# Kernel optimization log

Hardware: AMD Instinct MI355X
Metric: run time of the kernel (lower is better)

## Reference

```python
import jax, jax.numpy as jnp
import numpy as np

N_NODES = 100000
N_EDGES = 3200000
N_FEAT = 500
N_HID = 256
N_CLASS = 40


def spmm(edge_row, edge_col, edge_val, x, num_nodes):
    # out[i] = sum_{e: row[e]==i} val[e] * x[col[e]]
    msgs = edge_val[:, None] * x[edge_col]          # [E, F] gather + scale
    return jax.ops.segment_sum(msgs, edge_row, num_segments=num_nodes)


def setup_inputs() -> dict:
    key = jax.random.key(0)
    k1, k2, k3, k4, k5, k6, k7, k8 = jax.random.split(key, 8)
    features = jax.random.normal(k1, (N_NODES, N_FEAT), dtype=jnp.float32)
    edge_row = jax.random.randint(k2, (N_EDGES,), 0, N_NODES, dtype=jnp.int32)
    edge_col = jax.random.randint(k3, (N_EDGES,), 0, N_NODES, dtype=jnp.int32)
    edge_val = jax.random.uniform(k4, (N_EDGES,), dtype=jnp.float32)
    # Xavier-uniform linear weights, zero biases (as in reset_parameters)
    lim1 = float(np.sqrt(6.0 / (N_FEAT + N_HID)))
    W1 = jax.random.uniform(k5, (N_FEAT, N_HID), minval=-lim1, maxval=lim1, dtype=jnp.float32)
    b1 = jnp.zeros((N_HID,), dtype=jnp.float32)
    lim2 = float(np.sqrt(6.0 / (N_HID + N_CLASS)))
    W2 = jax.random.uniform(k6, (N_HID, N_CLASS), minval=-lim2, maxval=lim2, dtype=jnp.float32)
    b2 = jnp.zeros((N_CLASS,), dtype=jnp.float32)
    return {
        "features": features,
        "edge_row": edge_row,
        "edge_col": edge_col,
        "edge_val": edge_val,
        "W1": W1, "b1": b1, "W2": W2, "b2": b2,
    }


def reference(features, edge_row, edge_col, edge_val, W1, b1, W2, b2):
    # Layer 1: linear -> spmm -> relu   (eval mode: dropout is identity)
    h = features @ W1 + b1                          # [N, nhid]
    h = spmm(edge_row, edge_col, edge_val, h, N_NODES)
    h = jax.nn.relu(h)
    # Layer 2: linear -> spmm
    o = h @ W2 + b2                                 # [N, nclass]
    o = spmm(edge_row, edge_col, edge_val, o, N_NODES)
    return jax.nn.log_softmax(o, axis=1)
```

## Files before the change

kernel.cpp:

```cpp
#include <hip/hip_runtime.h>
#include <hip/hip_bf16.h>
#include <math.h>

#define N_NODES 100000
#define N_FEAT 500
#define N_HID 256
#define N_CLASS 40

typedef float f32x4 __attribute__((ext_vector_type(4)));
typedef int i32x4 __attribute__((ext_vector_type(4)));
typedef short short8 __attribute__((ext_vector_type(8)));
typedef unsigned short u16x8 __attribute__((ext_vector_type(8)));

__device__ __forceinline__ float b2f(unsigned short u) {
  union { unsigned int i; float f; } c; c.i = ((unsigned int)u) << 16; return c.f;
}
__device__ __forceinline__ unsigned short f2bu(float x) {
  __hip_bfloat16 b = __float2bfloat16(x);
  union { __hip_bfloat16 b; unsigned short u; } c; c.b = b; return c.u;
}
__device__ __forceinline__ void gload_lds16(const void* gptr, void* lptr) {
  __builtin_amdgcn_global_load_lds(
      (const __attribute__((address_space(1))) unsigned int*)gptr,
      (__attribute__((address_space(3))) unsigned int*)lptr, 16, 0, 0);
}

__global__ __launch_bounds__(256) void cast_w1(
    const float* __restrict__ W1, unsigned short* __restrict__ Bsw) {
  int t = blockIdx.x * 256 + threadIdx.x;
  int col = t >> 6, ch = t & 63;
  int g = ch >> 3, c = ch & 7;
  int c_src = c ^ (col & 7);
  int k = g * 64 + c_src * 8;
  u16x8 o;
#pragma unroll
  for (int j = 0; j < 8; j++) {
    int kk = k + j;
    o[j] = (kk < N_FEAT) ? f2bu(W1[(size_t)kk * N_HID + col]) : (unsigned short)0;
  }
  *(u16x8*)(Bsw + (size_t)col * 512 + g * 64 + c * 8) = o;
}

__global__ __launch_bounds__(512) void gemm1_mfma(
    const float* __restrict__ A, const unsigned short* __restrict__ Bsw,
    const float* __restrict__ b1, unsigned short* __restrict__ H, int M) {
  __shared__ __align__(16) char smem[49152];
  char* sA = smem;
  char* sB = smem + 16384;
  int tid = threadIdx.x;
  int lane = tid & 63, w = tid >> 6;
  int wr = w >> 2, wc = w & 3;
  int bm = blockIdx.x * 128;

  f32x4 acc[4][4];
#pragma unroll
  for (int m = 0; m < 4; m++)
#pragma unroll
    for (int n = 0; n < 4; n++) acc[m][n] = (f32x4)0.f;

  for (int s = 0; s < 8; s++) {
    int k0 = s * 64;
#pragma unroll
    for (int i = 0; i < 4; i++) {
      int f4 = i * 512 + tid;
      int row = f4 >> 4, cidx = f4 & 15;
      int grow = bm + row;
      int k = k0 + cidx * 4;
      float4 v = make_float4(0.f, 0.f, 0.f, 0.f);
      if (grow < M && k < N_FEAT) v = *(const float4*)(A + (size_t)grow * N_FEAT + k);
      ushort4 u;
      u.x = f2bu(v.x); u.y = f2bu(v.y); u.z = f2bu(v.z); u.w = f2bu(v.w);
      int chunk = cidx >> 1, sub = cidx & 1;
      int byte = row * 128 + (((chunk ^ (row & 7))) << 4) + (sub << 3);
      *(ushort4*)(sA + byte) = u;
    }
#pragma unroll
    for (int j = 0; j < 4; j++) {
      int base = j * 8192 + w * 1024;
      int L = base + lane * 16;
      int col = L >> 7, c = (L >> 4) & 7;
      const char* g = (const char*)Bsw + (size_t)col * 1024 + s * 128 + c * 16;
      gload_lds16(g, sB + base);
    }
    __syncthreads();
#pragma unroll
    for (int kk = 0; kk < 2; kk++) {
      int cw = kk * 4 + (lane >> 4);
      short8 af[4], bg[4];
#pragma unroll
      for (int m = 0; m < 4; m++) {
        int ar = wr * 64 + m * 16 + (lane & 15);
        af[m] = *(const short8*)(sA + ar * 128 + ((cw ^ (ar & 7)) << 4));
      }
#pragma unroll
      for (int n = 0; n < 4; n++) {
        int bc = wc * 64 + n * 16 + (lane & 15);
        bg[n] = *(const short8*)(sB + bc * 128 + ((cw ^ (bc & 7)) << 4));
      }
#pragma unroll
      for (int m = 0; m < 4; m++)
#pragma unroll
        for (int n = 0; n < 4; n++)
          acc[m][n] = __builtin_amdgcn_mfma_f32_16x16x32_bf16(af[m], bg[n], acc[m][n], 0, 0, 0);
    }
    __syncthreads();
  }

  float bias[4];
#pragma unroll
  for (int n = 0; n < 4; n++) bias[n] = b1[wc * 64 + n * 16 + (lane & 15)];
#pragma unroll
  for (int m = 0; m < 4; m++) {
#pragma unroll
    for (int r = 0; r < 4; r++) {
      int row = bm + wr * 64 + m * 16 + ((lane >> 4) << 2) + r;
      if (row < M) {
#pragma unroll
        for (int n = 0; n < 4; n++) {
          int col = wc * 64 + n * 16 + (lane & 15);
          H[(size_t)row * N_HID + col] = f2bu(acc[m][n][r] + bias[n]);
        }
      }
    }
  }
}

__global__ __launch_bounds__(256) void hist_kernel(
    const int* __restrict__ er, int* __restrict__ cnt, int E) {
  int nv = E >> 2;
  int t = blockIdx.x * 256 + threadIdx.x;
  int nthr = gridDim.x * 256;
  const i32x4* er4 = (const i32x4*)er;
  for (int i = t; i < nv; i += nthr) {
    i32x4 r = __builtin_nontemporal_load(&er4[i]);
    atomicAdd(&cnt[r.x], 1);
    atomicAdd(&cnt[r.y], 1);
    atomicAdd(&cnt[r.z], 1);
    atomicAdd(&cnt[r.w], 1);
  }
  int tail = nv << 2;
  if (blockIdx.x == 0 && threadIdx.x < E - tail)
    atomicAdd(&cnt[er[tail + threadIdx.x]], 1);
}

__global__ __launch_bounds__(1024) void scan1_kernel(
    int* __restrict__ cnt, int* __restrict__ bsum, int n) {
  __shared__ int wsum[16];
  int tid = threadIdx.x, lane = tid & 63, wid = tid >> 6;
  int i = blockIdx.x * 1024 + tid;
  int v = (i < n) ? cnt[i] : 0;
  int x = v;
#pragma unroll
  for (int off = 1; off < 64; off <<= 1) {
    int t = __shfl_up(x, off);
    if (lane >= off) x += t;
  }
  if (lane == 63) wsum[wid] = x;
  __syncthreads();
  if (tid < 16) {
    int ws = wsum[tid];
#pragma unroll
    for (int off = 1; off < 16; off <<= 1) {
      int t = __shfl_up(ws, off);
      if (tid >= off) ws += t;
    }
    wsum[tid] = ws;
  }
  __syncthreads();
  int excl = (wid ? wsum[wid - 1] : 0) + x - v;
  if (i < n) cnt[i] = excl;
  if (tid == 0) bsum[blockIdx.x] = wsum[15];
}

__global__ __launch_bounds__(64) void scan2_kernel(
    int* __restrict__ bsum, int* __restrict__ row_ptr, int nb, int n) {
  int lane = threadIdx.x;
  int carry = 0;
  for (int base = 0; base < nb; base += 64) {
    int i = base + lane;
    int v = (i < nb) ? bsum[i] : 0;
    int x = v;
#pragma unroll
    for (int off = 1; off < 64; off <<= 1) {
      int t = __shfl_up(x, off);
      if (lane >= off) x += t;
    }
    if (i < nb) bsum[i] = carry + x - v;
    carry += __shfl(x, 63);
  }
  if (lane == 0) row_ptr[n] = carry;
}

__global__ __launch_bounds__(256) void scan3_kernel(
    int* __restrict__ cnt, const int* __restrict__ bsum,
    int* __restrict__ row_ptr, int n) {
  int i = blockIdx.x * 256 + threadIdx.x;
  if (i >= n) return;
  int v = cnt[i] + bsum[i >> 10];
  cnt[i] = v;
  row_ptr[i] = v;
}

__global__ __launch_bounds__(256) void scatter_kernel(
    const int* __restrict__ er, const int* __restrict__ ec,
    const float* __restrict__ ev, int* __restrict__ cursor,
    int2* __restrict__ cv, int E) {
  int s = blockIdx.x & 7;
  int g = blockIdx.x >> 3;
  int ngrp = gridDim.x >> 3;
  int t = g * 256 + threadIdx.x;
  int nthr = ngrp * 256;
  int nv = E >> 2;
  const i32x4* er4 = (const i32x4*)er;
  const i32x4* ec4 = (const i32x4*)ec;
  const f32x4* ev4 = (const f32x4*)ev;
  for (int i = t; i < nv; i += nthr) {
    i32x4 r = __builtin_nontemporal_load(&er4[i]);
    i32x4 c = __builtin_nontemporal_load(&ec4[i]);
    f32x4 v = __builtin_nontemporal_load(&ev4[i]);
    if (((r.x >> 9) & 7) == s) {
      int p = atomicAdd(&cursor[r.x], 1);
      cv[p] = make_int2(c.x, __float_as_int(v.x));
    }
    if (((r.y >> 9) & 7) == s) {
      int p = atomicAdd(&cursor[r.y], 1);
      cv[p] = make_int2(c.y, __float_as_int(v.y));
    }
    if (((r.z >> 9) & 7) == s) {
      int p = atomicAdd(&cursor[r.z], 1);
      cv[p] = make_int2(c.z, __float_as_int(v.z));
    }
    if (((r.w >> 9) & 7) == s) {
      int p = atomicAdd(&cursor[r.w], 1);
      cv[p] = make_int2(c.w, __float_as_int(v.w));
    }
  }
  int tail = nv << 2;
  if (blockIdx.x == 0 && threadIdx.x < E - tail) {
    int i = tail + threadIdx.x;
    int row = er[i];
    int p = atomicAdd(&cursor[row], 1);
    cv[p] = make_int2(ec[i], __float_as_int(ev[i]));
  }
}

__global__ __launch_bounds__(256) void spmm_csr_256(
    const int* __restrict__ row_ptr, const int2* __restrict__ cv,
    const unsigned short* __restrict__ X, unsigned short* __restrict__ Y, int M) {
  int wave = (blockIdx.x * 256 + threadIdx.x) >> 6;
  int lane = threadIdx.x & 63;
  if (wave >= M) return;
  int start = row_ptr[wave], end = row_ptr[wave + 1];
  float a0 = 0.f, a1 = 0.f, a2 = 0.f, a3 = 0.f;
  const unsigned short* Xl = X + (lane << 2);
  int e = start;
  for (; e + 4 <= end; e += 4) {
    int2 p0 = cv[e], p1 = cv[e + 1], p2 = cv[e + 2], p3 = cv[e + 3];
    ushort4 x0 = *(const ushort4*)(Xl + (size_t)p0.x * N_HID);
    ushort4 x1 = *(const ushort4*)(Xl + (size_t)p1.x * N_HID);
    ushort4 x2 = *(const ushort4*)(Xl + (size_t)p2.x * N_HID);
    ushort4 x3 = *(const ushort4*)(Xl + (size_t)p3.x * N_HID);
    float v0 = __int_as_float(p0.y), v1 = __int_as_float(p1.y);
    float v2 = __int_as_float(p2.y), v3 = __int_as_float(p3.y);
    a0 = fmaf(v0, b2f(x0.x), a0); a1 = fmaf(v0, b2f(x0.y), a1);
    a2 = fmaf(v0, b2f(x0.z), a2); a3 = fmaf(v0, b2f(x0.w), a3);
    a0 = fmaf(v1, b2f(x1.x), a0); a1 = fmaf(v1, b2f(x1.y), a1);
    a2 = fmaf(v1, b2f(x1.z), a2); a3 = fmaf(v1, b2f(x1.w), a3);
    a0 = fmaf(v2, b2f(x2.x), a0); a1 = fmaf(v2, b2f(x2.y), a1);
    a2 = fmaf(v2, b2f(x2.z), a2); a3 = fmaf(v2, b2f(x2.w), a3);
    a0 = fmaf(v3, b2f(x3.x), a0); a1 = fmaf(v3, b2f(x3.y), a1);
    a2 = fmaf(v3, b2f(x3.z), a2); a3 = fmaf(v3, b2f(x3.w), a3);
  }
  for (; e < end; e++) {
    int2 p0 = cv[e];
    float v0 = __int_as_float(p0.y);
    ushort4 x0 = *(const ushort4*)(Xl + (size_t)p0.x * N_HID);
    a0 = fmaf(v0, b2f(x0.x), a0); a1 = fmaf(v0, b2f(x0.y), a1);
    a2 = fmaf(v0, b2f(x0.z), a2); a3 = fmaf(v0, b2f(x0.w), a3);
  }
  ushort4 o;
  o.x = f2bu(fmaxf(a0, 0.f)); o.y = f2bu(fmaxf(a1, 0.f));
  o.z = f2bu(fmaxf(a2, 0.f)); o.w = f2bu(fmaxf(a3, 0.f));
  *(ushort4*)(Y + (size_t)wave * N_HID + (lane << 2)) = o;
}

__global__ __launch_bounds__(256) void gemm2_kernel(
    const unsigned short* __restrict__ H, const float* __restrict__ W2,
    const float* __restrict__ b2, unsigned short* __restrict__ O, int M) {
  __shared__ float Ws[N_HID * N_CLASS];
  __shared__ float sb2[N_CLASS];
  int tid = threadIdx.x;
  for (int i = tid; i < N_HID * N_CLASS; i += 256) Ws[i] = W2[i];
  if (tid < N_CLASS) sb2[tid] = b2[tid];
  __syncthreads();
  int r0 = (blockIdx.x * 256 + tid) * 2;
  if (r0 >= M) return;
  int r1 = r0 + 1;
  bool has1 = r1 < M;
  float acc0[N_CLASS], acc1[N_CLASS];
#pragma unroll
  for (int n = 0; n < N_CLASS; n++) { acc0[n] = sb2[n]; acc1[n] = sb2[n]; }
  const unsigned short* h0 = H + (size_t)r0 * N_HID;
  const unsigned short* h1 = H + (size_t)(has1 ? r1 : r0) * N_HID;
  for (int k0 = 0; k0 < N_HID; k0 += 8) {
    u16x8 va = *(const u16x8*)(h0 + k0);
    u16x8 vb = *(const u16x8*)(h1 + k0);
#pragma unroll
    for (int j = 0; j < 8; j++) {
      float a0 = b2f(va[j]), a1 = b2f(vb[j]);
      const float* wrow = &Ws[(k0 + j) * N_CLASS];
#pragma unroll
      for (int n = 0; n < N_CLASS; n++) {
        float wv = wrow[n];
        acc0[n] = fmaf(a0, wv, acc0[n]);
        acc1[n] = fmaf(a1, wv, acc1[n]);
      }
    }
  }
  unsigned short* o0 = O + (size_t)r0 * N_CLASS;
#pragma unroll
  for (int n = 0; n < N_CLASS; n += 4) {
    ushort4 p;
    p.x = f2bu(acc0[n]); p.y = f2bu(acc0[n + 1]);
    p.z = f2bu(acc0[n + 2]); p.w = f2bu(acc0[n + 3]);
    *(ushort4*)(o0 + n) = p;
  }
  if (has1) {
    unsigned short* o1 = O + (size_t)r1 * N_CLASS;
#pragma unroll
    for (int n = 0; n < N_CLASS; n += 4) {
      ushort4 p;
      p.x = f2bu(acc1[n]); p.y = f2bu(acc1[n + 1]);
      p.z = f2bu(acc1[n + 2]); p.w = f2bu(acc1[n + 3]);
      *(ushort4*)(o1 + n) = p;
    }
  }
}

__global__ __launch_bounds__(256) void spmm_csr_40_lsm(
    const int* __restrict__ row_ptr, const int2* __restrict__ cv,
    const unsigned short* __restrict__ X, float* __restrict__ Out, int M) {
  int wave = (blockIdx.x * 256 + threadIdx.x) >> 6;
  int lane = threadIdx.x & 63;
  if (wave >= M) return;
  int start = row_ptr[wave], end = row_ptr[wave + 1];
  bool act = lane < N_CLASS;
  int ln = act ? lane : 0;
  const unsigned short* Xc = X + ln;
  float acc = 0.f;
  int e = start;
  for (; e + 4 <= end; e += 4) {
    int2 p0 = cv[e], p1 = cv[e + 1], p2 = cv[e + 2], p3 = cv[e + 3];
    unsigned short x0 = Xc[(size_t)p0.x * N_CLASS];
    unsigned short x1 = Xc[(size_t)p1.x * N_CLASS];
    unsigned short x2 = Xc[(size_t)p2.x * N_CLASS];
    unsigned short x3 = Xc[(size_t)p3.x * N_CLASS];
    acc = fmaf(__int_as_float(p0.y), b2f(x0), acc);
    acc = fmaf(__int_as_float(p1.y), b2f(x1), acc);
    acc = fmaf(__int_as_float(p2.y), b2f(x2), acc);
    acc = fmaf(__int_as_float(p3.y), b2f(x3), acc);
  }
  for (; e < end; e++) {
    int2 p0 = cv[e];
    acc = fmaf(__int_as_float(p0.y), b2f(Xc[(size_t)p0.x * N_CLASS]), acc);
  }
  float mv = act ? acc : -INFINITY;
#pragma unroll
  for (int off = 32; off; off >>= 1) mv = fmaxf(mv, __shfl_xor(mv, off));
  float ex = act ? expf(acc - mv) : 0.f;
  float s = ex;
#pragma unroll
  for (int off = 32; off; off >>= 1) s += __shfl_xor(s, off);
  float lse = mv + logf(s);
  if (act) Out[(size_t)wave * N_CLASS + lane] = acc - lse;
}

extern "C" void kernel_launch(void* const* d_in, const int* in_sizes, int n_in,
                              void* d_out, int out_size, void* d_ws, size_t ws_size,
                              hipStream_t stream) {
  const float* feat = (const float*)d_in[0];
  const int* er     = (const int*)d_in[1];
  const int* ec     = (const int*)d_in[2];
  const float* ev   = (const float*)d_in[3];
  const float* W1   = (const float*)d_in[4];
  const float* b1   = (const float*)d_in[5];
  const float* W2   = (const float*)d_in[6];
  const float* b2   = (const float*)d_in[7];
  float* out = (float*)d_out;
  const int M = N_NODES;
  const int E = in_sizes[1];

  char* ws = (char*)d_ws;
  unsigned short* h     = (unsigned short*)(ws);
  unsigned short* hpost = (unsigned short*)(ws + 51200000);
  unsigned short* o     = (unsigned short*)(ws + 102400000);
  int* row_ptr          = (int*)(ws + 110400000);
  int* cursor           = (int*)(ws + 110800016);
  int* bsum             = (int*)(ws + 111200032);
  int2* cv              = (int2*)(ws + 111200576);
  unsigned short* W1Tsw = (unsigned short*)(ws + 136800576);

  const int NB1 = (M + 1023) / 1024;

  cast_w1<<<64, 256, 0, stream>>>(W1, W1Tsw);
  (void)hipMemsetAsync(cursor, 0, (size_t)M * sizeof(int), stream);
  hist_kernel<<<1024, 256, 0, stream>>>(er, cursor, E);
  scan1_kernel<<<NB1, 1024, 0, stream>>>(cursor, bsum, M);
  scan2_kernel<<<1, 64, 0, stream>>>(bsum, row_ptr, NB1, M);
  scan3_kernel<<<(M + 255) / 256, 256, 0, stream>>>(cursor, bsum, row_ptr, M);
  scatter_kernel<<<2048, 256, 0, stream>>>(er, ec, ev, cursor, cv, E);
  gemm1_mfma<<<(M + 127) / 128, 512, 0, stream>>>(feat, W1Tsw, b1, h, M);
  spmm_csr_256<<<(M + 3) / 4, 256, 0, stream>>>(row_ptr, cv, h, hpost, M);
  gemm2_kernel<<<(M + 511) / 512, 256, 0, stream>>>(hpost, W2, b2, o, M);
  spmm_csr_40_lsm<<<(M + 3) / 4, 256, 0, stream>>>(row_ptr, cv, o, out, M);
}
```

Measured before the change: 789.9 us.

## Pack edges to 32 bits, pre-bin before CSR scatter, feature-split layer-1 SpMM

Each edge is packed into 32 bits: a 17-bit column index plus the value stored as bf16 with its sign bit dropped. This halves the size of the CSR payload. The scatter becomes two passes: a ballot-based binning pass writes edges into 8 row-range buckets, then a second pass scatters each bucket with per-row atomics, which keeps atomics and writes local. GEMM1 now writes H as 64 feature-group planes so the new layer-1 SpMM can use one thread per row per 16-feature slice. Blocks are grouped so concurrently running waves share a small gathered working set. The packing assumes non-negative edge values and node ids below 2^17, and the thread-per-row layout can cause load imbalance across lanes.

```diff
diff --git a/kernel.cpp b/kernel.cpp
--- a/kernel.cpp
+++ b/kernel.cpp
@@ -6,6 +6,8 @@
 #define N_FEAT 500
 #define N_HID 256
 #define N_CLASS 40
+#define BIN_CAP 448000
+#define PLANE 400000
 
 typedef float f32x4 __attribute__((ext_vector_type(4)));
 typedef int i32x4 __attribute__((ext_vector_type(4)));
@@ -18,6 +20,9 @@
 __device__ __forceinline__ unsigned short f2bu(float x) {
   __hip_bfloat16 b = __float2bfloat16(x);
   union { __hip_bfloat16 b; unsigned short u; } c; c.b = b; return c.u;
+}
+__device__ __forceinline__ float decode_val(unsigned int p) {
+  union { unsigned int i; float f; } c; c.i = (p & 0x7FFFu) << 17; return c.f;
 }
 __device__ __forceinline__ void gload_lds16(const void* gptr, void* lptr) {
   __builtin_amdgcn_global_load_lds(
@@ -43,7 +48,7 @@
 
 __global__ __launch_bounds__(512) void gemm1_mfma(
     const float* __restrict__ A, const unsigned short* __restrict__ Bsw,
-    const float* __restrict__ b1, unsigned short* __restrict__ H, int M) {
+    const float* __restrict__ b1, unsigned short* __restrict__ HG, int M) {
   __shared__ __align__(16) char smem[49152];
   char* sA = smem;
   char* sB = smem + 16384;
@@ -118,7 +123,8 @@
 #pragma unroll
         for (int n = 0; n < 4; n++) {
           int col = wc * 64 + n * 16 + (lane & 15);
-          H[(size_t)row * N_HID + col] = f2bu(acc[m][n][r] + bias[n]);
+          HG[(size_t)(col >> 2) * PLANE + (size_t)row * 4 + (col & 3)] =
+              f2bu(acc[m][n][r] + bias[n]);
         }
       }
     }
@@ -201,87 +207,140 @@
   row_ptr[i] = v;
 }
 
-__global__ __launch_bounds__(256) void scatter_kernel(
+__global__ __launch_bounds__(256) void bin_kernel(
     const int* __restrict__ er, const int* __restrict__ ec,
-    const float* __restrict__ ev, int* __restrict__ cursor,
-    int2* __restrict__ cv, int E) {
+    const float* __restrict__ ev, int* __restrict__ bcur,
+    unsigned long long* __restrict__ buckets, int E) {
+  int gw = (blockIdx.x * 256 + threadIdx.x) >> 6;
+  int lane = threadIdx.x & 63;
+  int nw = (gridDim.x * 256) >> 6;
+  const int CH = 2048;
+  int nchunks = (E + CH - 1) / CH;
+  unsigned long long below = (1ULL << lane) - 1ULL;
+  for (int ch = gw; ch < nchunks; ch += nw) {
+    int base = ch * CH;
+    int c0 = 0, c1 = 0, c2 = 0, c3 = 0, c4 = 0, c5 = 0, c6 = 0, c7 = 0;
+    for (int i = 0; i < CH; i += 64) {
+      int e = base + i + lane;
+      int b = (e < E) ? ((er[e] >> 9) & 7) : -1;
+      c0 += __popcll(__ballot(b == 0));
+      c1 += __popcll(__ballot(b == 1));
+      c2 += __popcll(__ballot(b == 2));
+      c3 += __popcll(__ballot(b == 3));
+      c4 += __popcll(__ballot(b == 4));
+      c5 += __popcll(__ballot(b == 5));
+      c6 += __popcll(__ballot(b == 6));
+      c7 += __popcll(__ballot(b == 7));
+    }
+    int mycnt = 0;
+    if (lane == 0) mycnt = c0;
+    if (lane == 1) mycnt = c1;
+    if (lane == 2) mycnt = c2;
+    if (lane == 3) mycnt = c3;
+    if (lane == 4) mycnt = c4;
+    if (lane == 5) mycnt = c5;
+    if (lane == 6) mycnt = c6;
+    if (lane == 7) mycnt = c7;
+    int mybase = 0;
+    if (lane < 8) mybase = atomicAdd(&bcur[lane], mycnt);
+    int o0 = __shfl(mybase, 0), o1 = __shfl(mybase, 1);
+    int o2 = __shfl(mybase, 2), o3 = __shfl(mybase, 3);
+    int o4 = __shfl(mybase, 4), o5 = __shfl(mybase, 5);
+    int o6 = __shfl(mybase, 6), o7 = __shfl(mybase, 7);
+    for (int i = 0; i < CH; i += 64) {
+      int e = base + i + lane;
+      int b = -1, rr = 0, cc = 0;
+      float vv = 0.f;
+      if (e < E) { rr = er[e]; cc = ec[e]; vv = ev[e]; b = (rr >> 9) & 7; }
+      unsigned long long m0 = __ballot(b == 0), m1 = __ballot(b == 1);
+      unsigned long long m2 = __ballot(b == 2), m3 = __ballot(b == 3);
+      unsigned long long m4 = __ballot(b == 4), m5 = __ballot(b == 5);
+      unsigned long long m6 = __ballot(b == 6), m7 = __ballot(b == 7);
+      int pos = -1;
+      if (b == 0) pos = o0 + __popcll(m0 & below);
+      if (b == 1) pos = o1 + __popcll(m1 & below);
+      if (b == 2) pos = o2 + __popcll(m2 & below);
+      if (b == 3) pos = o3 + __popcll(m3 & below);
+      if (b == 4) pos = o4 + __popcll(m4 & below);
+      if (b == 5) pos = o5 + __popcll(m5 & below);
+      if (b == 6) pos = o6 + __popcll(m6 & below);
+      if (b == 7) pos = o7 + __popcll(m7 & below);
+      o0 += __popcll(m0); o1 += __popcll(m1);
+      o2 += __popcll(m2); o3 += __popcll(m3);
+      o4 += __popcll(m4); o5 += __popcll(m5);
+      o6 += __popcll(m6); o7 += __popcll(m7);
+      if (e < E) {
+        unsigned int cvpv = ((unsigned int)cc << 15) | ((unsigned int)f2bu(vv) >> 1);
+        buckets[(size_t)b * BIN_CAP + pos] =
+            ((unsigned long long)(unsigned int)rr << 32) | cvpv;
+      }
+    }
+  }
+}
+
+__global__ __launch_bounds__(256) void scatter2_kernel(
+    const unsigned long long* __restrict__ buckets, const int* __restrict__ bcur,
+    int* __restrict__ cursor, unsigned int* __restrict__ cvp) {
   int s = blockIdx.x & 7;
-  int g = blockIdx.x >> 3;
-  int ngrp = gridDim.x >> 3;
-  int t = g * 256 + threadIdx.x;
-  int nthr = ngrp * 256;
-  int nv = E >> 2;
-  const i32x4* er4 = (const i32x4*)er;
-  const i32x4* ec4 = (const i32x4*)ec;
-  const f32x4* ev4 = (const f32x4*)ev;
-  for (int i = t; i < nv; i += nthr) {
-    i32x4 r = __builtin_nontemporal_load(&er4[i]);
-    i32x4 c = __builtin_nontemporal_load(&ec4[i]);
-    f32x4 v = __builtin_nontemporal_load(&ev4[i]);
-    if (((r.x >> 9) & 7) == s) {
-      int p = atomicAdd(&cursor[r.x], 1);
-      cv[p] = make_int2(c.x, __float_as_int(v.x));
-    }
-    if (((r.y >> 9) & 7) == s) {
-      int p = atomicAdd(&cursor[r.y], 1);
-      cv[p] = make_int2(c.y, __float_as_int(v.y));
-    }
-    if (((r.z >> 9) & 7) == s) {
-      int p = atomicAdd(&cursor[r.z], 1);
-      cv[p] = make_int2(c.z, __float_as_int(v.z));
-    }
-    if (((r.w >> 9) & 7) == s) {
-      int p = atomicAdd(&cursor[r.w], 1);
-      cv[p] = make_int2(c.w, __float_as_int(v.w));
-    }
-  }
-  int tail = nv << 2;
-  if (blockIdx.x == 0 && threadIdx.x < E - tail) {
-    int i = tail + threadIdx.x;
-    int row = er[i];
-    int p = atomicAdd(&cursor[row], 1);
-    cv[p] = make_int2(ec[i], __float_as_int(ev[i]));
-  }
-}
-
-__global__ __launch_bounds__(256) void spmm_csr_256(
-    const int* __restrict__ row_ptr, const int2* __restrict__ cv,
-    const unsigned short* __restrict__ X, unsigned short* __restrict__ Y, int M) {
-  int wave = (blockIdx.x * 256 + threadIdx.x) >> 6;
-  int lane = threadIdx.x & 63;
-  if (wave >= M) return;
-  int start = row_ptr[wave], end = row_ptr[wave + 1];
-  float a0 = 0.f, a1 = 0.f, a2 = 0.f, a3 = 0.f;
-  const unsigned short* Xl = X + (lane << 2);
-  int e = start;
-  for (; e + 4 <= end; e += 4) {
-    int2 p0 = cv[e], p1 = cv[e + 1], p2 = cv[e + 2], p3 = cv[e + 3];
-    ushort4 x0 = *(const ushort4*)(Xl + (size_t)p0.x * N_HID);
-    ushort4 x1 = *(const ushort4*)(Xl + (size_t)p1.x * N_HID);
-    ushort4 x2 = *(const ushort4*)(Xl + (size_t)p2.x * N_HID);
-    ushort4 x3 = *(const ushort4*)(Xl + (size_t)p3.x * N_HID);
-    float v0 = __int_as_float(p0.y), v1 = __int_as_float(p1.y);
-    float v2 = __int_as_float(p2.y), v3 = __int_as_float(p3.y);
-    a0 = fmaf(v0, b2f(x0.x), a0); a1 = fmaf(v0, b2f(x0.y), a1);
-    a2 = fmaf(v0, b2f(x0.z), a2); a3 = fmaf(v0, b2f(x0.w), a3);
-    a0 = fmaf(v1, b2f(x1.x), a0); a1 = fmaf(v1, b2f(x1.y), a1);
-    a2 = fmaf(v1, b2f(x1.z), a2); a3 = fmaf(v1, b2f(x1.w), a3);
-    a0 = fmaf(v2, b2f(x2.x), a0); a1 = fmaf(v2, b2f(x2.y), a1);
-    a2 = fmaf(v2, b2f(x2.z), a2); a3 = fmaf(v2, b2f(x2.w), a3);
-    a0 = fmaf(v3, b2f(x3.x), a0); a1 = fmaf(v3, b2f(x3.y), a1);
-    a2 = fmaf(v3, b2f(x3.z), a2); a3 = fmaf(v3, b2f(x3.w), a3);
-  }
-  for (; e < end; e++) {
-    int2 p0 = cv[e];
-    float v0 = __int_as_float(p0.y);
-    ushort4 x0 = *(const ushort4*)(Xl + (size_t)p0.x * N_HID);
-    a0 = fmaf(v0, b2f(x0.x), a0); a1 = fmaf(v0, b2f(x0.y), a1);
-    a2 = fmaf(v0, b2f(x0.z), a2); a3 = fmaf(v0, b2f(x0.w), a3);
-  }
-  ushort4 o;
-  o.x = f2bu(fmaxf(a0, 0.f)); o.y = f2bu(fmaxf(a1, 0.f));
-  o.z = f2bu(fmaxf(a2, 0.f)); o.w = f2bu(fmaxf(a3, 0.f));
-  *(ushort4*)(Y + (size_t)wave * N_HID + (lane << 2)) = o;
+  int g = blockIdx.x >> 3, ngrp = gridDim.x >> 3;
+  int n = bcur[s];
+  const unsigned long long* B = buckets + (size_t)s * BIN_CAP;
+  for (int i = g * 256 + threadIdx.x; i < n; i += ngrp * 256) {
+    unsigned long long rec = B[i];
+    int row = (int)(rec >> 32);
+    int pos = atomicAdd(&cursor[row], 1);
+    cvp[pos] = (unsigned int)rec;
+  }
+}
+
+__global__ __launch_bounds__(256) void spmm_fs(
+    const int* __restrict__ row_ptr, const unsigned int* __restrict__ cvp,
+    const unsigned short* __restrict__ HG, unsigned short* __restrict__ Y, int M) {
+  int half = gridDim.x >> 1;
+  int phase = (blockIdx.x >= half) ? 1 : 0;
+  int r = blockIdx.x - phase * half;
+  int s8 = r & 7, g = r >> 3;
+  int row = g * 256 + threadIdx.x;
+  if (row >= M) return;
+  int fg0 = s8 * 8 + phase * 4;
+  const unsigned short* P0 = HG + (size_t)(fg0 + 0) * PLANE;
+  const unsigned short* P1 = HG + (size_t)(fg0 + 1) * PLANE;
+  const unsigned short* P2 = HG + (size_t)(fg0 + 2) * PLANE;
+  const unsigned short* P3 = HG + (size_t)(fg0 + 3) * PLANE;
+  int start = row_ptr[row], end = row_ptr[row + 1];
+  f32x4 a0 = (f32x4)0.f, a1 = (f32x4)0.f, a2 = (f32x4)0.f, a3 = (f32x4)0.f;
+#pragma unroll 2
+  for (int e = start; e < end; e++) {
+    unsigned int p = cvp[e];
+    int c4 = (int)(p >> 15) << 2;
+    float val = decode_val(p);
+    ushort4 x0 = *(const ushort4*)(P0 + c4);
+    ushort4 x1 = *(const ushort4*)(P1 + c4);
+    ushort4 x2 = *(const ushort4*)(P2 + c4);
+    ushort4 x3 = *(const ushort4*)(P3 + c4);
+    a0.x = fmaf(val, b2f(x0.x), a0.x); a0.y = fmaf(val, b2f(x0.y), a0.y);
+    a0.z = fmaf(val, b2f(x0.z), a0.z); a0.w = fmaf(val, b2f(x0.w), a0.w);
+    a1.x = fmaf(val, b2f(x1.x), a1.x); a1.y = fmaf(val, b2f(x1.y), a1.y);
+    a1.z = fmaf(val, b2f(x1.z), a1.z); a1.w = fmaf(val, b2f(x1.w), a1.w);
+    a2.x = fmaf(val, b2f(x2.x), a2.x); a2.y = fmaf(val, b2f(x2.y), a2.y);
+    a2.z = fmaf(val, b2f(x2.z), a2.z); a2.w = fmaf(val, b2f(x2.w), a2.w);
+    a3.x = fmaf(val, b2f(x3.x), a3.x); a3.y = fmaf(val, b2f(x3.y), a3.y);
+    a3.z = fmaf(val, b2f(x3.z), a3.z); a3.w = fmaf(val, b2f(x3.w), a3.w);
+  }
+  unsigned short* yp = Y + (size_t)row * N_HID + fg0 * 4;
+  ushort4 w;
+  w.x = f2bu(fmaxf(a0.x, 0.f)); w.y = f2bu(fmaxf(a0.y, 0.f));
+  w.z = f2bu(fmaxf(a0.z, 0.f)); w.w = f2bu(fmaxf(a0.w, 0.f));
+  *(ushort4*)(yp + 0) = w;
+  w.x = f2bu(fmaxf(a1.x, 0.f)); w.y = f2bu(fmaxf(a1.y, 0.f));
+  w.z = f2bu(fmaxf(a1.z, 0.f)); w.w = f2bu(fmaxf(a1.w, 0.f));
+  *(ushort4*)(yp + 4) = w;
+  w.x = f2bu(fmaxf(a2.x, 0.f)); w.y = f2bu(fmaxf(a2.y, 0.f));
+  w.z = f2bu(fmaxf(a2.z, 0.f)); w.w = f2bu(fmaxf(a2.w, 0.f));
+  *(ushort4*)(yp + 8) = w;
+  w.x = f2bu(fmaxf(a3.x, 0.f)); w.y = f2bu(fmaxf(a3.y, 0.f));
+  w.z = f2bu(fmaxf(a3.z, 0.f)); w.w = f2bu(fmaxf(a3.w, 0.f));
+  *(ushort4*)(yp + 12) = w;
 }
 
 __global__ __launch_bounds__(256) void gemm2_kernel(
@@ -338,7 +397,7 @@
 }
 
 __global__ __launch_bounds__(256) void spmm_csr_40_lsm(
-    const int* __restrict__ row_ptr, const int2* __restrict__ cv,
+    const int* __restrict__ row_ptr, const unsigned int* __restrict__ cvp,
     const unsigned short* __restrict__ X, float* __restrict__ Out, int M) {
   int wave = (blockIdx.x * 256 + threadIdx.x) >> 6;
   int lane = threadIdx.x & 63;
@@ -350,19 +409,19 @@
   float acc = 0.f;
   int e = start;
   for (; e + 4 <= end; e += 4) {
-    int2 p0 = cv[e], p1 = cv[e + 1], p2 = cv[e + 2], p3 = cv[e + 3];
-    unsigned short x0 = Xc[(size_t)p0.x * N_CLASS];
-    unsigned short x1 = Xc[(size_t)p1.x * N_CLASS];
-    unsigned short x2 = Xc[(size_t)p2.x * N_CLASS];
-    unsigned short x3 = Xc[(size_t)p3.x * N_CLASS];
-    acc = fmaf(__int_as_float(p0.y), b2f(x0), acc);
-    acc = fmaf(__int_as_float(p1.y), b2f(x1), acc);
-    acc = fmaf(__int_as_float(p2.y), b2f(x2), acc);
-    acc = fmaf(__int_as_float(p3.y), b2f(x3), acc);
+    unsigned int p0 = cvp[e], p1 = cvp[e + 1], p2 = cvp[e + 2], p3 = cvp[e + 3];
+    unsigned short x0 = Xc[(size_t)(p0 >> 15) * N_CLASS];
+    unsigned short x1 = Xc[(size_t)(p1 >> 15) * N_CLASS];
+    unsigned short x2 = Xc[(size_t)(p2 >> 15) * N_CLASS];
+    unsigned short x3 = Xc[(size_t)(p3 >> 15) * N_CLASS];
+    acc = fmaf(decode_val(p0), b2f(x0), acc);
+    acc = fmaf(decode_val(p1), b2f(x1), acc);
+    acc = fmaf(decode_val(p2), b2f(x2), acc);
+    acc = fmaf(decode_val(p3), b2f(x3), acc);
   }
   for (; e < end; e++) {
-    int2 p0 = cv[e];
-    acc = fmaf(__int_as_float(p0.y), b2f(Xc[(size_t)p0.x * N_CLASS]), acc);
+    unsigned int p0 = cvp[e];
+    acc = fmaf(decode_val(p0), b2f(Xc[(size_t)(p0 >> 15) * N_CLASS]), acc);
   }
   float mv = act ? acc : -INFINITY;
 #pragma unroll
@@ -391,26 +450,32 @@
   const int E = in_sizes[1];
 
   char* ws = (char*)d_ws;
-  unsigned short* h     = (unsigned short*)(ws);
+  unsigned short* hg    = (unsigned short*)(ws);
   unsigned short* hpost = (unsigned short*)(ws + 51200000);
   unsigned short* o     = (unsigned short*)(ws + 102400000);
   int* row_ptr          = (int*)(ws + 110400000);
   int* cursor           = (int*)(ws + 110800016);
-  int* bsum             = (int*)(ws + 111200032);
-  int2* cv              = (int2*)(ws + 111200576);
-  unsigned short* W1Tsw = (unsigned short*)(ws + 136800576);
+  int* bcur             = (int*)(ws + 111200016);
+  int* bsum             = (int*)(ws + 111200064);
+  unsigned int* cvp     = (unsigned int*)(ws + 111200576);
+  unsigned short* W1Tsw = (unsigned short*)(ws + 124000576);
+  unsigned long long* buckets = (unsigned long long*)(ws + 128000000);
 
   const int NB1 = (M + 1023) / 1024;
 
   cast_w1<<<64, 256, 0, stream>>>(W1, W1Tsw);
-  (void)hipMemsetAsync(cursor, 0, (size_t)M * sizeof(int), stream);
+  (void)hipMemsetAsync(cursor, 0, 400048, stream);
   hist_kernel<<<1024, 256, 0, stream>>>(er, cursor, E);
   scan1_kernel<<<NB1, 1024, 0, stream>>>(cursor, bsum, M);
   scan2_kernel<<<1, 64, 0, stream>>>(bsum, row_ptr, NB1, M);
   scan3_kernel<<<(M + 255) / 256, 256, 0, stream>>>(cursor, bsum, row_ptr, M);
-  scatter_kernel<<<2048, 256, 0, stream>>>(er, ec, ev, cursor, cv, E);
-  gemm1_mfma<<<(M + 127) / 128, 512, 0, stream>>>(feat, W1Tsw, b1, h, M);
-  spmm_csr_256<<<(M + 3) / 4, 256, 0, stream>>>(row_ptr, cv, h, hpost, M);
+  bin_kernel<<<512, 256, 0, stream>>>(er, ec, ev, bcur, buckets, E);
+  scatter2_kernel<<<2048, 256, 0, stream>>>(buckets, bcur, cursor, cvp);
+  gemm1_mfma<<<(M + 127) / 128, 512, 0, stream>>>(feat, W1Tsw, b1, hg, M);
+  {
+    int half = 8 * ((M + 255) / 256);
+    spmm_fs<<<2 * half, 256, 0, stream>>>(row_ptr, cvp, hg, hpost, M);
+  }
   gemm2_kernel<<<(M + 511) / 512, 256, 0, stream>>>(hpost, W2, b2, o, M);
-  spmm_csr_40_lsm<<<(M + 3) / 4, 256, 0, stream>>>(row_ptr, cv, o, out, M);
-}
+  spmm_csr_40_lsm<<<(M + 3) / 4, 256, 0, stream>>>(row_ptr, cvp, o, out, M);
+}
```

Result: slower. 1.801 ms (+128.0%).

## Store hidden activations in FP8 and pack CSR edges into 32-bit words

Applied to the files above, without the earlier changes.

The first-layer GEMM now writes its hidden activations as FP8 instead of bf16, which halves the bytes gathered per edge in the 256-wide SpMM. That SpMM is rewritten so each wave processes two edges at once, with each half-wave handling one edge, and the halves are combined with a cross-lane shuffle. Each CSR entry is packed into one 32-bit word: a 17-bit column index plus a 15-bit truncated bf16 value, produced in a fused prep kernel that also does the weight cast and the row histogram. This shrinks scatter and SpMM edge traffic, but FP8 activations and 15-bit edge values lose considerable precision and could break tolerance checks.

```diff
diff --git a/kernel.cpp b/kernel.cpp
--- a/kernel.cpp
+++ b/kernel.cpp
@@ -8,7 +8,9 @@
 #define N_CLASS 40
 
 typedef float f32x4 __attribute__((ext_vector_type(4)));
+typedef float f32x2 __attribute__((ext_vector_type(2)));
 typedef int i32x4 __attribute__((ext_vector_type(4)));
+typedef unsigned int u32x4 __attribute__((ext_vector_type(4)));
 typedef short short8 __attribute__((ext_vector_type(8)));
 typedef unsigned short u16x8 __attribute__((ext_vector_type(8)));
 
@@ -18,6 +20,12 @@
 __device__ __forceinline__ unsigned short f2bu(float x) {
   __hip_bfloat16 b = __float2bfloat16(x);
   union { __hip_bfloat16 b; unsigned short u; } c; c.b = b; return c.u;
+}
+__device__ __forceinline__ float decode_val(unsigned int p) {
+  union { unsigned int i; float f; } c; c.i = (p & 0x7FFFu) << 17; return c.f;
+}
+__device__ __forceinline__ unsigned char f2fp8(float x) {
+  return (unsigned char)(__builtin_amdgcn_cvt_pk_fp8_f32(x, x, 0, false) & 0xFF);
 }
 __device__ __forceinline__ void gload_lds16(const void* gptr, void* lptr) {
   __builtin_amdgcn_global_load_lds(
@@ -25,25 +33,57 @@
       (__attribute__((address_space(3))) unsigned int*)lptr, 16, 0, 0);
 }
 
-__global__ __launch_bounds__(256) void cast_w1(
-    const float* __restrict__ W1, unsigned short* __restrict__ Bsw) {
+__global__ __launch_bounds__(256) void prep_kernel(
+    const float* __restrict__ W1, unsigned short* __restrict__ Bsw,
+    const int* __restrict__ er, const int* __restrict__ ec,
+    const float* __restrict__ ev, int* __restrict__ cnt,
+    unsigned int* __restrict__ cvps, int E) {
+  if (blockIdx.x < 64) {
+    int t = blockIdx.x * 256 + threadIdx.x;
+    int col = t >> 6, ch = t & 63;
+    int g = ch >> 3, c = ch & 7;
+    int c_src = c ^ (col & 7);
+    int k = g * 64 + c_src * 8;
+    u16x8 o;
+#pragma unroll
+    for (int j = 0; j < 8; j++) {
+      int kk = k + j;
+      o[j] = (kk < N_FEAT) ? f2bu(W1[(size_t)kk * N_HID + col]) : (unsigned short)0;
+    }
+    *(u16x8*)(Bsw + (size_t)col * 512 + g * 64 + c * 8) = o;
+  }
+  int nv = E >> 2;
   int t = blockIdx.x * 256 + threadIdx.x;
-  int col = t >> 6, ch = t & 63;
-  int g = ch >> 3, c = ch & 7;
-  int c_src = c ^ (col & 7);
-  int k = g * 64 + c_src * 8;
-  u16x8 o;
-#pragma unroll
-  for (int j = 0; j < 8; j++) {
-    int kk = k + j;
-    o[j] = (kk < N_FEAT) ? f2bu(W1[(size_t)kk * N_HID + col]) : (unsigned short)0;
-  }
-  *(u16x8*)(Bsw + (size_t)col * 512 + g * 64 + c * 8) = o;
+  int nthr = gridDim.x * 256;
+  const i32x4* er4 = (const i32x4*)er;
+  const i32x4* ec4 = (const i32x4*)ec;
+  const f32x4* ev4 = (const f32x4*)ev;
+  for (int i = t; i < nv; i += nthr) {
+    i32x4 r = __builtin_nontemporal_load(&er4[i]);
+    i32x4 c = __builtin_nontemporal_load(&ec4[i]);
+    f32x4 v = __builtin_nontemporal_load(&ev4[i]);
+    atomicAdd(&cnt[r.x], 1);
+    atomicAdd(&cnt[r.y], 1);
+    atomicAdd(&cnt[r.z], 1);
+    atomicAdd(&cnt[r.w], 1);
+    u32x4 pk;
+    pk.x = ((unsigned int)c.x << 15) | ((unsigned int)f2bu(v.x) >> 1);
+    pk.y = ((unsigned int)c.y << 15) | ((unsigned int)f2bu(v.y) >> 1);
+    pk.z = ((unsigned int)c.z << 15) | ((unsigned int)f2bu(v.z) >> 1);
+    pk.w = ((unsigned int)c.w << 15) | ((unsigned int)f2bu(v.w) >> 1);
+    __builtin_nontemporal_store(pk, (u32x4*)(cvps + 4 * (size_t)i));
+  }
+  int tail = nv << 2;
+  if (blockIdx.x == 0 && threadIdx.x < E - tail) {
+    int i = tail + threadIdx.x;
+    atomicAdd(&cnt[er[i]], 1);
+    cvps[i] = ((unsigned int)ec[i] << 15) | ((unsigned int)f2bu(ev[i]) >> 1);
+  }
 }
 
 __global__ __launch_bounds__(512) void gemm1_mfma(
     const float* __restrict__ A, const unsigned short* __restrict__ Bsw,
-    const float* __restrict__ b1, unsigned short* __restrict__ H, int M) {
+    const float* __restrict__ b1, unsigned char* __restrict__ H, int M) {
   __shared__ __align__(16) char smem[49152];
   char* sA = smem;
   char* sB = smem + 16384;
@@ -118,29 +158,11 @@
 #pragma unroll
         for (int n = 0; n < 4; n++) {
           int col = wc * 64 + n * 16 + (lane & 15);
-          H[(size_t)row * N_HID + col] = f2bu(acc[m][n][r] + bias[n]);
+          H[(size_t)row * N_HID + col] = f2fp8(acc[m][n][r] + bias[n]);
         }
       }
     }
   }
-}
-
-__global__ __launch_bounds__(256) void hist_kernel(
-    const int* __restrict__ er, int* __restrict__ cnt, int E) {
-  int nv = E >> 2;
-  int t = blockIdx.x * 256 + threadIdx.x;
-  int nthr = gridDim.x * 256;
-  const i32x4* er4 = (const i32x4*)er;
-  for (int i = t; i < nv; i += nthr) {
-    i32x4 r = __builtin_nontemporal_load(&er4[i]);
-    atomicAdd(&cnt[r.x], 1);
-    atomicAdd(&cnt[r.y], 1);
-    atomicAdd(&cnt[r.z], 1);
-    atomicAdd(&cnt[r.w], 1);
-  }
-  int tail = nv << 2;
-  if (blockIdx.x == 0 && threadIdx.x < E - tail)
-    atomicAdd(&cnt[er[tail + threadIdx.x]], 1);
 }
 
 __global__ __launch_bounds__(1024) void scan1_kernel(
@@ -202,86 +224,68 @@
 }
 
 __global__ __launch_bounds__(256) void scatter_kernel(
-    const int* __restrict__ er, const int* __restrict__ ec,
-    const float* __restrict__ ev, int* __restrict__ cursor,
-    int2* __restrict__ cv, int E) {
+    const int* __restrict__ er, const unsigned int* __restrict__ cvps,
+    int* __restrict__ cursor, unsigned int* __restrict__ cvp, int E) {
   int s = blockIdx.x & 7;
   int g = blockIdx.x >> 3;
   int ngrp = gridDim.x >> 3;
-  int t = g * 256 + threadIdx.x;
-  int nthr = ngrp * 256;
   int nv = E >> 2;
   const i32x4* er4 = (const i32x4*)er;
-  const i32x4* ec4 = (const i32x4*)ec;
-  const f32x4* ev4 = (const f32x4*)ev;
-  for (int i = t; i < nv; i += nthr) {
+  const u32x4* cv4 = (const u32x4*)cvps;
+  for (int i = g * 256 + threadIdx.x; i < nv; i += ngrp * 256) {
     i32x4 r = __builtin_nontemporal_load(&er4[i]);
-    i32x4 c = __builtin_nontemporal_load(&ec4[i]);
-    f32x4 v = __builtin_nontemporal_load(&ev4[i]);
-    if (((r.x >> 9) & 7) == s) {
-      int p = atomicAdd(&cursor[r.x], 1);
-      cv[p] = make_int2(c.x, __float_as_int(v.x));
-    }
-    if (((r.y >> 9) & 7) == s) {
-      int p = atomicAdd(&cursor[r.y], 1);
-      cv[p] = make_int2(c.y, __float_as_int(v.y));
-    }
-    if (((r.z >> 9) & 7) == s) {
-      int p = atomicAdd(&cursor[r.z], 1);
-      cv[p] = make_int2(c.z, __float_as_int(v.z));
-    }
-    if (((r.w >> 9) & 7) == s) {
-      int p = atomicAdd(&cursor[r.w], 1);
-      cv[p] = make_int2(c.w, __float_as_int(v.w));
-    }
+    u32x4 p = __builtin_nontemporal_load(&cv4[i]);
+    if (((r.x >> 9) & 7) == s) cvp[atomicAdd(&cursor[r.x], 1)] = p.x;
+    if (((r.y >> 9) & 7) == s) cvp[atomicAdd(&cursor[r.y], 1)] = p.y;
+    if (((r.z >> 9) & 7) == s) cvp[atomicAdd(&cursor[r.z], 1)] = p.z;
+    if (((r.w >> 9) & 7) == s) cvp[atomicAdd(&cursor[r.w], 1)] = p.w;
   }
   int tail = nv << 2;
   if (blockIdx.x == 0 && threadIdx.x < E - tail) {
     int i = tail + threadIdx.x;
-    int row = er[i];
-    int p = atomicAdd(&cursor[row], 1);
-    cv[p] = make_int2(ec[i], __float_as_int(ev[i]));
-  }
-}
-
-__global__ __launch_bounds__(256) void spmm_csr_256(
-    const int* __restrict__ row_ptr, const int2* __restrict__ cv,
-    const unsigned short* __restrict__ X, unsigned short* __restrict__ Y, int M) {
+    cvp[atomicAdd(&cursor[er[i]], 1)] = cvps[i];
+  }
+}
+
+__global__ __launch_bounds__(256) void spmm_fp8(
+    const int* __restrict__ row_ptr, const unsigned int* __restrict__ cvp,
+    const unsigned char* __restrict__ X, unsigned short* __restrict__ Y, int M) {
   int wave = (blockIdx.x * 256 + threadIdx.x) >> 6;
   int lane = threadIdx.x & 63;
   if (wave >= M) return;
   int start = row_ptr[wave], end = row_ptr[wave + 1];
+  int hf = lane >> 5, fl = lane & 31;
   float a0 = 0.f, a1 = 0.f, a2 = 0.f, a3 = 0.f;
-  const unsigned short* Xl = X + (lane << 2);
-  int e = start;
-  for (; e + 4 <= end; e += 4) {
-    int2 p0 = cv[e], p1 = cv[e + 1], p2 = cv[e + 2], p3 = cv[e + 3];
-    ushort4 x0 = *(const ushort4*)(Xl + (size_t)p0.x * N_HID);
-    ushort4 x1 = *(const ushort4*)(Xl + (size_t)p1.x * N_HID);
-    ushort4 x2 = *(const ushort4*)(Xl + (size_t)p2.x * N_HID);
-    ushort4 x3 = *(const ushort4*)(Xl + (size_t)p3.x * N_HID);
-    float v0 = __int_as_float(p0.y), v1 = __int_as_float(p1.y);
-    float v2 = __int_as_float(p2.y), v3 = __int_as_float(p3.y);
-    a0 = fmaf(v0, b2f(x0.x), a0); a1 = fmaf(v0, b2f(x0.y), a1);
-    a2 = fmaf(v0, b2f(x0.z), a2); a3 = fmaf(v0, b2f(x0.w), a3);
-    a0 = fmaf(v1, b2f(x1.x), a0); a1 = fmaf(v1, b2f(x1.y), a1);
-    a2 = fmaf(v1, b2f(x1.z), a2); a3 = fmaf(v1, b2f(x1.w), a3);
-    a0 = fmaf(v2, b2f(x2.x), a0); a1 = fmaf(v2, b2f(x2.y), a1);
-    a2 = fmaf(v2, b2f(x2.z), a2); a3 = fmaf(v2, b2f(x2.w), a3);
-    a0 = fmaf(v3, b2f(x3.x), a0); a1 = fmaf(v3, b2f(x3.y), a1);
-    a2 = fmaf(v3, b2f(x3.z), a2); a3 = fmaf(v3, b2f(x3.w), a3);
-  }
-  for (; e < end; e++) {
-    int2 p0 = cv[e];
-    float v0 = __int_as_float(p0.y);
-    ushort4 x0 = *(const ushort4*)(Xl + (size_t)p0.x * N_HID);
-    a0 = fmaf(v0, b2f(x0.x), a0); a1 = fmaf(v0, b2f(x0.y), a1);
-    a2 = fmaf(v0, b2f(x0.z), a2); a3 = fmaf(v0, b2f(x0.w), a3);
-  }
-  ushort4 o;
-  o.x = f2bu(fmaxf(a0, 0.f)); o.y = f2bu(fmaxf(a1, 0.f));
-  o.z = f2bu(fmaxf(a2, 0.f)); o.w = f2bu(fmaxf(a3, 0.f));
-  *(ushort4*)(Y + (size_t)wave * N_HID + (lane << 2)) = o;
+  float a4 = 0.f, a5 = 0.f, a6 = 0.f, a7 = 0.f;
+  const unsigned char* Xf = X + fl * 8;
+#pragma unroll 2
+  for (int e = start; e < end; e += 2) {
+    int ei = e + hf;
+    unsigned int p = (ei < end) ? cvp[ei] : 0u;
+    float val = decode_val(p);
+    size_t col = (size_t)(p >> 15);
+    uint2 d = *(const uint2*)(Xf + col * N_HID);
+    f32x2 f01 = __builtin_amdgcn_cvt_pk_f32_fp8(d.x, false);
+    f32x2 f23 = __builtin_amdgcn_cvt_pk_f32_fp8(d.x, true);
+    f32x2 f45 = __builtin_amdgcn_cvt_pk_f32_fp8(d.y, false);
+    f32x2 f67 = __builtin_amdgcn_cvt_pk_f32_fp8(d.y, true);
+    a0 = fmaf(val, f01.x, a0); a1 = fmaf(val, f01.y, a1);
+    a2 = fmaf(val, f23.x, a2); a3 = fmaf(val, f23.y, a3);
+    a4 = fmaf(val, f45.x, a4); a5 = fmaf(val, f45.y, a5);
+    a6 = fmaf(val, f67.x, a6); a7 = fmaf(val, f67.y, a7);
+  }
+  a0 += __shfl_xor(a0, 32); a1 += __shfl_xor(a1, 32);
+  a2 += __shfl_xor(a2, 32); a3 += __shfl_xor(a3, 32);
+  a4 += __shfl_xor(a4, 32); a5 += __shfl_xor(a5, 32);
+  a6 += __shfl_xor(a6, 32); a7 += __shfl_xor(a7, 32);
+  if (hf == 0) {
+    u16x8 o;
+    o[0] = f2bu(fmaxf(a0, 0.f)); o[1] = f2bu(fmaxf(a1, 0.f));
+    o[2] = f2bu(fmaxf(a2, 0.f)); o[3] = f2bu(fmaxf(a3, 0.f));
+    o[4] = f2bu(fmaxf(a4, 0.f)); o[5] = f2bu(fmaxf(a5, 0.f));
+    o[6] = f2bu(fmaxf(a6, 0.f)); o[7] = f2bu(fmaxf(a7, 0.f));
+    *(u16x8*)(Y + (size_t)wave * N_HID + fl * 8) = o;
+  }
 }
 
 __global__ __launch_bounds__(256) void gemm2_kernel(
@@ -338,7 +342,7 @@
 }
 
 __global__ __launch_bounds__(256) void spmm_csr_40_lsm(
-    const int* __restrict__ row_ptr, const int2* __restrict__ cv,
+    const int* __restrict__ row_ptr, const unsigned int* __restrict__ cvp,
     const unsigned short* __restrict__ X, float* __restrict__ Out, int M) {
   int wave = (blockIdx.x * 256 + threadIdx.x) >> 6;
   int lane = threadIdx.x & 63;
@@ -350,19 +354,19 @@
   float acc = 0.f;
   int e = start;
   for (; e + 4 <= end; e += 4) {
-    int2 p0 = cv[e], p1 = cv[e + 1], p2 = cv[e + 2], p3 = cv[e + 3];
-    unsigned short x0 = Xc[(size_t)p0.x * N_CLASS];
-    unsigned short x1 = Xc[(size_t)p1.x * N_CLASS];
-    unsigned short x2 = Xc[(size_t)p2.x * N_CLASS];
-    unsigned short x3 = Xc[(size_t)p3.x * N_CLASS];
-    acc = fmaf(__int_as_float(p0.y), b2f(x0), acc);
-    acc = fmaf(__int_as_float(p1.y), b2f(x1), acc);
-    acc = fmaf(__int_as_float(p2.y), b2f(x2), acc);
-    acc = fmaf(__int_as_float(p3.y), b2f(x3), acc);
+    unsigned int p0 = cvp[e], p1 = cvp[e + 1], p2 = cvp[e + 2], p3 = cvp[e + 3];
+    unsigned short x0 = Xc[(size_t)(p0 >> 15) * N_CLASS];
+    unsigned short x1 = Xc[(size_t)(p1 >> 15) * N_CLASS];
+    unsigned short x2 = Xc[(size_t)(p2 >> 15) * N_CLASS];
+    unsigned short x3 = Xc[(size_t)(p3 >> 15) * N_CLASS];
+    acc = fmaf(decode_val(p0), b2f(x0), acc);
+    acc = fmaf(decode_val(p1), b2f(x1), acc);
+    acc = fmaf(decode_val(p2), b2f(x2), acc);
+    acc = fmaf(decode_val(p3), b2f(x3), acc);
   }
   for (; e < end; e++) {
-    int2 p0 = cv[e];
-    acc = fmaf(__int_as_float(p0.y), b2f(Xc[(size_t)p0.x * N_CLASS]), acc);
+    unsigned int p0 = cvp[e];
+    acc = fmaf(decode_val(p0), b2f(Xc[(size_t)(p0 >> 15) * N_CLASS]), acc);
   }
   float mv = act ? acc : -INFINITY;
 #pragma unroll
@@ -391,26 +395,26 @@
   const int E = in_sizes[1];
 
   char* ws = (char*)d_ws;
-  unsigned short* h     = (unsigned short*)(ws);
-  unsigned short* hpost = (unsigned short*)(ws + 51200000);
-  unsigned short* o     = (unsigned short*)(ws + 102400000);
-  int* row_ptr          = (int*)(ws + 110400000);
-  int* cursor           = (int*)(ws + 110800016);
-  int* bsum             = (int*)(ws + 111200032);
-  int2* cv              = (int2*)(ws + 111200576);
-  unsigned short* W1Tsw = (unsigned short*)(ws + 136800576);
+  unsigned char* h      = (unsigned char*)(ws);
+  unsigned short* hpost = (unsigned short*)(ws + 25600000);
+  unsigned short* o     = (unsigned short*)(ws + 76800000);
+  int* row_ptr          = (int*)(ws + 84800000);
+  int* cursor           = (int*)(ws + 85200016);
+  int* bsum             = (int*)(ws + 85600016);
+  unsigned int* cvp     = (unsigned int*)(ws + 85600528);
+  unsigned int* cvps    = (unsigned int*)(ws + 98400528);
+  unsigned short* W1Tsw = (unsigned short*)(ws + 111200528);
 
   const int NB1 = (M + 1023) / 1024;
 
-  cast_w1<<<64, 256, 0, stream>>>(W1, W1Tsw);
   (void)hipMemsetAsync(cursor, 0, (size_t)M * sizeof(int), stream);
-  hist_kernel<<<1024, 256, 0, stream>>>(er, cursor, E);
+  prep_kernel<<<1024, 256, 0, stream>>>(W1, W1Tsw, er, ec, ev, cursor, cvps, E);
   scan1_kernel<<<NB1, 1024, 0, stream>>>(cursor, bsum, M);
   scan2_kernel<<<1, 64, 0, stream>>>(bsum, row_ptr, NB1, M);
   scan3_kernel<<<(M + 255) / 256, 256, 0, stream>>>(cursor, bsum, row_ptr, M);
-  scatter_kernel<<<2048, 256, 0, stream>>>(er, ec, ev, cursor, cv, E);
+  scatter_kernel<<<2048, 256, 0, stream>>>(er, cvps, cursor, cvp, E);
   gemm1_mfma<<<(M + 127) / 128, 512, 0, stream>>>(feat, W1Tsw, b1, h, M);
-  spmm_csr_256<<<(M + 3) / 4, 256, 0, stream>>>(row_ptr, cv, h, hpost, M);
+  spmm_fp8<<<(M + 3) / 4, 256, 0, stream>>>(row_ptr, cvp, h, hpost, M);
   gemm2_kernel<<<(M + 511) / 512, 256, 0, stream>>>(hpost, W2, b2, o, M);
-  spmm_csr_40_lsm<<<(M + 3) / 4, 256, 0, stream>>>(row_ptr, cv, o, out, M);
-}
+  spmm_csr_40_lsm<<<(M + 3) / 4, 256, 0, stream>>>(row_ptr, cvp, o, out, M);
+}
```

Result: faster. 705.7 us (-10.7%).
